# Kernel optimization log

Measured on AMD Instinct MI355X. Metric: run time of the kernel, lower is better.

Reference implementation:

```python
import jax, jax.numpy as jnp
import numpy as np

B, S, IN, H, D, M, OUT = 1, 4096, 2048, 2048, 1024, 65536, 2048
TOP_K = 3
EPS = 1e-12  # F.normalize eps


def setup_inputs() -> dict:
    key = jax.random.key(0)
    ks = jax.random.split(key, 13)
    def g(k, shape, scale):
        return jax.random.normal(k, shape, dtype=jnp.float32) * scale
    return {
        "x": g(ks[0], (B, S, IN), 1.0),
        "W1": g(ks[1], (IN, H), (1.0 / IN) ** 0.5),
        "b1": g(ks[2], (H,), 0.01),
        "W2": g(ks[3], (H, H), (1.0 / H) ** 0.5),
        "b2": g(ks[4], (H,), 0.01),
        "Wq": g(ks[5], (H, D), (1.0 / H) ** 0.5),
        "bq": g(ks[6], (D,), 0.01),
        "Wout": g(ks[7], (H + D, OUT), (1.0 / (H + D)) ** 0.5),
        "bout": g(ks[8], (OUT,), 0.01),
        "keys": g(ks[9], (M, D), 1.0),
        "values": g(ks[10], (M, D), 1.0),
        "importance": jax.random.uniform(ks[11], (M,), dtype=jnp.float32),
    }


def _l2norm(v):
    n = jnp.sqrt(jnp.sum(v * v, axis=-1, keepdims=True))
    return v / jnp.maximum(n, EPS)


def reference(x, W1, b1, W2, b2, Wq, bq, Wout, bout, keys, values, importance):
    # controller: Linear -> ReLU -> Linear over flattened tokens
    h = jnp.maximum(x.reshape(-1, IN) @ W1 + b1, 0.0) @ W2 + b2  # [B*S, H]
    h = h.reshape(B, S, H)
    last_hidden = h[:, -1, :]                                    # [B=1, H]
    # query generation + cosine similarity against memory keys
    q = last_hidden @ Wq + bq                                    # [1, D]
    qn = _l2norm(q)
    kn = _l2norm(keys)                                           # [M, D]
    sims = (qn @ kn.T)[0]                                        # [M]
    weighted = sims * importance                                 # [M]
    top_vals, top_idx = jax.lax.top_k(weighted, TOP_K)
    attn = jax.nn.softmax(top_vals)                              # [K]
    retrieved = attn @ values[top_idx]                           # [D]
    combined = jnp.concatenate([last_hidden, retrieved[None, :]], axis=-1)  # [1, H+D]
    out = combined @ Wout + bout                                 # [1, OUT]
    return out
```

## Files before the change

### kernel.cpp

```cpp
#include <hip/hip_runtime.h>

#define FEPS 1e-12f

template<int RELU>
__global__ void gemv_atomic4(const float* __restrict__ v,
                             const float* __restrict__ W,
                             const float* __restrict__ bias,
                             float* __restrict__ out,
                             int C, int chunk) {
    int j = (blockIdx.x * 256 + threadIdx.x) * 4;
    int i0 = blockIdx.y * chunk;
    float4 acc = make_float4(0.f, 0.f, 0.f, 0.f);
    for (int i = i0; i < i0 + chunk; ++i) {
        float vi = v[i];
        if (RELU) vi = fmaxf(vi, 0.f);
        float4 w = *(const float4*)(W + (size_t)i * C + j);
        acc.x += vi * w.x; acc.y += vi * w.y;
        acc.z += vi * w.z; acc.w += vi * w.w;
    }
    if (blockIdx.y == 0) {
        float4 b = *(const float4*)(bias + j);
        acc.x += b.x; acc.y += b.y; acc.z += b.z; acc.w += b.w;
    }
    atomicAdd(&out[j + 0], acc.x);
    atomicAdd(&out[j + 1], acc.y);
    atomicAdd(&out[j + 2], acc.z);
    atomicAdd(&out[j + 3], acc.w);
}

__global__ void sims_top3(const float* __restrict__ q,
                          const float* __restrict__ keys,
                          const float* __restrict__ imp,
                          float* __restrict__ cand_val,
                          int* __restrict__ cand_idx) {
    __shared__ float qs[1024];
    __shared__ float wv[4 * 3];
    __shared__ int   wi[4 * 3];
    int t = threadIdx.x;
    #pragma unroll
    for (int p = 0; p < 4; ++p) qs[t + 256 * p] = q[t + 256 * p];
    __syncthreads();
    int wave = t >> 6, lane = t & 63;
    const float4* q4 = (const float4*)qs;
    float4 qv[4];
    #pragma unroll
    for (int p = 0; p < 4; ++p) qv[p] = q4[lane + 64 * p];

    float v0 = -INFINITY, v1 = -INFINITY, v2 = -INFINITY;
    int   i0 = -1, i1 = -1, i2 = -1;
    int mbase = blockIdx.x * 64 + wave * 16;
    for (int r = 0; r < 16; ++r) {
        int m = mbase + r;
        const float4* krow = (const float4*)(keys + (size_t)m * 1024);
        float dot = 0.f, sq = 0.f;
        #pragma unroll
        for (int p = 0; p < 4; ++p) {
            float4 k = krow[lane + 64 * p];
            dot += k.x * qv[p].x + k.y * qv[p].y + k.z * qv[p].z + k.w * qv[p].w;
            sq  += k.x * k.x + k.y * k.y + k.z * k.z + k.w * k.w;
        }
        #pragma unroll
        for (int off = 32; off; off >>= 1) {
            dot += __shfl_down(dot, off);
            sq  += __shfl_down(sq, off);
        }
        if (lane == 0) {
            float val = dot * imp[m] / fmaxf(sqrtf(sq), FEPS);
            if (val > v0)      { v2 = v1; i2 = i1; v1 = v0; i1 = i0; v0 = val; i0 = m; }
            else if (val > v1) { v2 = v1; i2 = i1; v1 = val; i1 = m; }
            else if (val > v2) { v2 = val; i2 = m; }
        }
    }
    if (lane == 0) {
        wv[wave * 3 + 0] = v0; wv[wave * 3 + 1] = v1; wv[wave * 3 + 2] = v2;
        wi[wave * 3 + 0] = i0; wi[wave * 3 + 1] = i1; wi[wave * 3 + 2] = i2;
    }
    __syncthreads();
    if (t == 0) {
        float a0 = -INFINITY, a1 = -INFINITY, a2 = -INFINITY;
        int   b0 = -1, b1 = -1, b2 = -1;
        for (int e = 0; e < 12; ++e) {
            float val = wv[e]; int idx = wi[e];
            if (val > a0)      { a2 = a1; b2 = b1; a1 = a0; b1 = b0; a0 = val; b0 = idx; }
            else if (val > a1) { a2 = a1; b2 = b1; a1 = val; b1 = idx; }
            else if (val > a2) { a2 = val; b2 = idx; }
        }
        cand_val[blockIdx.x * 3 + 0] = a0; cand_idx[blockIdx.x * 3 + 0] = b0;
        cand_val[blockIdx.x * 3 + 1] = a1; cand_idx[blockIdx.x * 3 + 1] = b1;
        cand_val[blockIdx.x * 3 + 2] = a2; cand_idx[blockIdx.x * 3 + 2] = b2;
    }
}

__global__ void finalize_retrieve(const float* __restrict__ q,
                                  const float* __restrict__ cand_val,
                                  const int* __restrict__ cand_idx,
                                  const float* __restrict__ values,
                                  float* __restrict__ retrieved) {
    __shared__ float red[1024];
    __shared__ float mv[3 * 1024];
    __shared__ int   mi[3 * 1024];
    __shared__ float s_attn[3];
    __shared__ int   s_idx[3];
    __shared__ float s_qden;
    int t = threadIdx.x;

    float qv = q[t];
    red[t] = qv * qv;
    __syncthreads();
    for (int s = 512; s > 0; s >>= 1) {
        if (t < s) red[t] += red[t + s];
        __syncthreads();
    }
    if (t == 0) s_qden = fmaxf(sqrtf(red[0]), FEPS);

    float v0 = -INFINITY, v1 = -INFINITY, v2 = -INFINITY;
    int   i0 = -1, i1 = -1, i2 = -1;
    #pragma unroll
    for (int k = 0; k < 3; ++k) {
        int c = t + (k << 10);
        float val = cand_val[c];
        int   idx = cand_idx[c];
        if (val > v0)      { v2 = v1; i2 = i1; v1 = v0; i1 = i0; v0 = val; i0 = idx; }
        else if (val > v1) { v2 = v1; i2 = i1; v1 = val; i1 = idx; }
        else if (val > v2) { v2 = val; i2 = idx; }
    }
    mv[t * 3 + 0] = v0; mv[t * 3 + 1] = v1; mv[t * 3 + 2] = v2;
    mi[t * 3 + 0] = i0; mi[t * 3 + 1] = i1; mi[t * 3 + 2] = i2;
    __syncthreads();

    for (int s = 512; s > 0; s >>= 1) {
        if (t < s) {
            float a0 = mv[t * 3], a1 = mv[t * 3 + 1], a2 = mv[t * 3 + 2];
            int   b0 = mi[t * 3], b1 = mi[t * 3 + 1], b2 = mi[t * 3 + 2];
            #pragma unroll
            for (int e = 0; e < 3; ++e) {
                float val = mv[(t + s) * 3 + e];
                int   idx = mi[(t + s) * 3 + e];
                if (val > a0)      { a2 = a1; b2 = b1; a1 = a0; b1 = b0; a0 = val; b0 = idx; }
                else if (val > a1) { a2 = a1; b2 = b1; a1 = val; b1 = idx; }
                else if (val > a2) { a2 = val; b2 = idx; }
            }
            mv[t * 3] = a0; mv[t * 3 + 1] = a1; mv[t * 3 + 2] = a2;
            mi[t * 3] = b0; mi[t * 3 + 1] = b1; mi[t * 3 + 2] = b2;
        }
        __syncthreads();
    }

    if (t == 0) {
        float qden = s_qden;
        float tv0 = mv[0] / qden, tv1 = mv[1] / qden, tv2 = mv[2] / qden;
        float mx = fmaxf(tv0, fmaxf(tv1, tv2));
        float e0 = expf(tv0 - mx), e1 = expf(tv1 - mx), e2 = expf(tv2 - mx);
        float sum = e0 + e1 + e2;
        s_attn[0] = e0 / sum; s_attn[1] = e1 / sum; s_attn[2] = e2 / sum;
        s_idx[0] = mi[0]; s_idx[1] = mi[1]; s_idx[2] = mi[2];
    }
    __syncthreads();

    float r = 0.0f;
    #pragma unroll
    for (int e = 0; e < 3; ++e)
        r += s_attn[e] * values[(size_t)s_idx[e] * 1024 + t];
    retrieved[t] = r;
}

extern "C" void kernel_launch(void* const* d_in, const int* in_sizes, int n_in,
                              void* d_out, int out_size, void* d_ws, size_t ws_size,
                              hipStream_t stream) {
    const float* x      = (const float*)d_in[0];
    const float* W1     = (const float*)d_in[1];
    const float* b1     = (const float*)d_in[2];
    const float* W2     = (const float*)d_in[3];
    const float* b2     = (const float*)d_in[4];
    const float* Wq     = (const float*)d_in[5];
    const float* bq     = (const float*)d_in[6];
    const float* Wout   = (const float*)d_in[7];
    const float* bout   = (const float*)d_in[8];
    const float* keys   = (const float*)d_in[9];
    const float* values = (const float*)d_in[10];
    const float* imp    = (const float*)d_in[11];
    float* out = (float*)d_out;
    float* ws  = (float*)d_ws;

    float* h1       = ws;
    float* comb     = ws + 2048;
    float* retr     = ws + 4096;
    float* q        = ws + 5120;
    float* cand_val = ws + 6144;
    int*   cand_idx = (int*)(ws + 9216);

    const float* xlast = x + (size_t)(4096 - 1) * 2048;

    hipMemsetAsync(d_ws, 0, 6144 * sizeof(float), stream);
    hipMemsetAsync(d_out, 0, (size_t)out_size * sizeof(float), stream);

    gemv_atomic4<0><<<dim3(2, 128), 256, 0, stream>>>(xlast, W1, b1, h1, 2048, 16);
    gemv_atomic4<1><<<dim3(2, 128), 256, 0, stream>>>(h1, W2, b2, comb, 2048, 16);
    gemv_atomic4<0><<<dim3(1, 128), 256, 0, stream>>>(comb, Wq, bq, q, 1024, 16);
    sims_top3<<<1024, 256, 0, stream>>>(q, keys, imp, cand_val, cand_idx);
    finalize_retrieve<<<1, 1024, 0, stream>>>(q, cand_val, cand_idx, values, retr);
    gemv_atomic4<0><<<dim3(2, 128), 256, 0, stream>>>(comb, Wout, bout, out, 2048, 24);
}
```

Measured before the change: 610.5 us.

## Fuse top-3 finalize into sims kernel via last-block counter, retune GEMV splits

Merges the separate single-block finalize/retrieve kernel into the similarity kernel: each block publishes its top-3 candidates, and the last block to finish (found with an atomic ticket counter) does the global top-3 merge, softmax, value gather and zeroing of the output buffer. This drops one kernel launch and one memset. The GEMV kernels now use a compile-time unrolled chunk with twice as many row-split blocks, and the key scan processes four rows at a time for more loads in flight. The cost is extra atomics and fences, and a serial tail on the last block.

After: 701.9 us. 1.15x slower.

```diff
diff --git a/kernel.cpp b/kernel.cpp
--- a/kernel.cpp
+++ b/kernel.cpp
@@ -2,21 +2,34 @@
 
 #define FEPS 1e-12f
 
-template<int RELU>
-__global__ void gemv_atomic4(const float* __restrict__ v,
-                             const float* __restrict__ W,
-                             const float* __restrict__ bias,
-                             float* __restrict__ out,
-                             int C, int chunk) {
+__device__ __forceinline__ void top3_insert(float val, int idx,
+                                            float& v0, float& v1, float& v2,
+                                            int& i0, int& i1, int& i2) {
+    if (val > v0)      { v2 = v1; i2 = i1; v1 = v0; i1 = i0; v0 = val; i0 = idx; }
+    else if (val > v1) { v2 = v1; i2 = i1; v1 = val; i1 = idx; }
+    else if (val > v2) { v2 = val; i2 = idx; }
+}
+
+template<int RELU, int CHUNK>
+__global__ __launch_bounds__(256)
+void gemv_atomic4(const float* __restrict__ v,
+                  const float* __restrict__ W,
+                  const float* __restrict__ bias,
+                  float* __restrict__ out,
+                  int C) {
     int j = (blockIdx.x * 256 + threadIdx.x) * 4;
-    int i0 = blockIdx.y * chunk;
+    int i0 = blockIdx.y * CHUNK;
     float4 acc = make_float4(0.f, 0.f, 0.f, 0.f);
-    for (int i = i0; i < i0 + chunk; ++i) {
+    #pragma unroll
+    for (int u = 0; u < CHUNK; ++u) {
+        int i = i0 + u;
         float vi = v[i];
         if (RELU) vi = fmaxf(vi, 0.f);
         float4 w = *(const float4*)(W + (size_t)i * C + j);
-        acc.x += vi * w.x; acc.y += vi * w.y;
-        acc.z += vi * w.z; acc.w += vi * w.w;
+        acc.x = fmaf(vi, w.x, acc.x);
+        acc.y = fmaf(vi, w.y, acc.y);
+        acc.z = fmaf(vi, w.z, acc.z);
+        acc.w = fmaf(vi, w.w, acc.w);
     }
     if (blockIdx.y == 0) {
         float4 b = *(const float4*)(bias + j);
@@ -28,14 +41,23 @@
     atomicAdd(&out[j + 3], acc.w);
 }
 
-__global__ void sims_top3(const float* __restrict__ q,
-                          const float* __restrict__ keys,
-                          const float* __restrict__ imp,
-                          float* __restrict__ cand_val,
-                          int* __restrict__ cand_idx) {
+__global__ __launch_bounds__(256)
+void sims_top3_fused(const float* __restrict__ q,
+                     const float* __restrict__ keys,
+                     const float* __restrict__ imp,
+                     const float* __restrict__ values,
+                     float* __restrict__ cand_val,
+                     int* __restrict__ cand_idx,
+                     unsigned* __restrict__ ctr,
+                     float* __restrict__ retr,
+                     float* __restrict__ out) {
     __shared__ float qs[1024];
     __shared__ float wv[4 * 3];
     __shared__ int   wi[4 * 3];
+    __shared__ float s_red[4];
+    __shared__ float s_attn[3];
+    __shared__ int   s_idx[3];
+    __shared__ int   s_last;
     int t = threadIdx.x;
     #pragma unroll
     for (int p = 0; p < 4; ++p) qs[t + 256 * p] = q[t + 256 * p];
@@ -49,26 +71,40 @@
     float v0 = -INFINITY, v1 = -INFINITY, v2 = -INFINITY;
     int   i0 = -1, i1 = -1, i2 = -1;
     int mbase = blockIdx.x * 64 + wave * 16;
-    for (int r = 0; r < 16; ++r) {
-        int m = mbase + r;
-        const float4* krow = (const float4*)(keys + (size_t)m * 1024);
-        float dot = 0.f, sq = 0.f;
+    for (int r = 0; r < 16; r += 4) {
+        float dot[4] = {0.f, 0.f, 0.f, 0.f};
+        float sq[4]  = {0.f, 0.f, 0.f, 0.f};
         #pragma unroll
-        for (int p = 0; p < 4; ++p) {
-            float4 k = krow[lane + 64 * p];
-            dot += k.x * qv[p].x + k.y * qv[p].y + k.z * qv[p].z + k.w * qv[p].w;
-            sq  += k.x * k.x + k.y * k.y + k.z * k.z + k.w * k.w;
+        for (int u = 0; u < 4; ++u) {
+            const float4* krow = (const float4*)(keys + (size_t)(mbase + r + u) * 1024);
+            #pragma unroll
+            for (int p = 0; p < 4; ++p) {
+                float4 k = krow[lane + 64 * p];
+                dot[u] = fmaf(k.x, qv[p].x, dot[u]);
+                dot[u] = fmaf(k.y, qv[p].y, dot[u]);
+                dot[u] = fmaf(k.z, qv[p].z, dot[u]);
+                dot[u] = fmaf(k.w, qv[p].w, dot[u]);
+                sq[u]  = fmaf(k.x, k.x, sq[u]);
+                sq[u]  = fmaf(k.y, k.y, sq[u]);
+                sq[u]  = fmaf(k.z, k.z, sq[u]);
+                sq[u]  = fmaf(k.w, k.w, sq[u]);
+            }
         }
         #pragma unroll
         for (int off = 32; off; off >>= 1) {
-            dot += __shfl_down(dot, off);
-            sq  += __shfl_down(sq, off);
+            #pragma unroll
+            for (int u = 0; u < 4; ++u) {
+                dot[u] += __shfl_down(dot[u], off);
+                sq[u]  += __shfl_down(sq[u], off);
+            }
         }
         if (lane == 0) {
-            float val = dot * imp[m] / fmaxf(sqrtf(sq), FEPS);
-            if (val > v0)      { v2 = v1; i2 = i1; v1 = v0; i1 = i0; v0 = val; i0 = m; }
-            else if (val > v1) { v2 = v1; i2 = i1; v1 = val; i1 = m; }
-            else if (val > v2) { v2 = val; i2 = m; }
+            #pragma unroll
+            for (int u = 0; u < 4; ++u) {
+                int m = mbase + r + u;
+                float val = dot[u] * imp[m] / fmaxf(sqrtf(sq[u]), FEPS);
+                top3_insert(val, m, v0, v1, v2, i0, i1, i2);
+            }
         }
     }
     if (lane == 0) {
@@ -79,89 +115,77 @@
     if (t == 0) {
         float a0 = -INFINITY, a1 = -INFINITY, a2 = -INFINITY;
         int   b0 = -1, b1 = -1, b2 = -1;
-        for (int e = 0; e < 12; ++e) {
-            float val = wv[e]; int idx = wi[e];
-            if (val > a0)      { a2 = a1; b2 = b1; a1 = a0; b1 = b0; a0 = val; b0 = idx; }
-            else if (val > a1) { a2 = a1; b2 = b1; a1 = val; b1 = idx; }
-            else if (val > a2) { a2 = val; b2 = idx; }
-        }
-        cand_val[blockIdx.x * 3 + 0] = a0; cand_idx[blockIdx.x * 3 + 0] = b0;
-        cand_val[blockIdx.x * 3 + 1] = a1; cand_idx[blockIdx.x * 3 + 1] = b1;
-        cand_val[blockIdx.x * 3 + 2] = a2; cand_idx[blockIdx.x * 3 + 2] = b2;
-    }
-}
-
-__global__ void finalize_retrieve(const float* __restrict__ q,
-                                  const float* __restrict__ cand_val,
-                                  const int* __restrict__ cand_idx,
-                                  const float* __restrict__ values,
-                                  float* __restrict__ retrieved) {
-    __shared__ float red[1024];
-    __shared__ float mv[3 * 1024];
-    __shared__ int   mi[3 * 1024];
-    __shared__ float s_attn[3];
-    __shared__ int   s_idx[3];
-    __shared__ float s_qden;
-    int t = threadIdx.x;
-
-    float qv = q[t];
-    red[t] = qv * qv;
-    __syncthreads();
-    for (int s = 512; s > 0; s >>= 1) {
-        if (t < s) red[t] += red[t + s];
-        __syncthreads();
-    }
-    if (t == 0) s_qden = fmaxf(sqrtf(red[0]), FEPS);
-
-    float v0 = -INFINITY, v1 = -INFINITY, v2 = -INFINITY;
-    int   i0 = -1, i1 = -1, i2 = -1;
-    #pragma unroll
-    for (int k = 0; k < 3; ++k) {
-        int c = t + (k << 10);
-        float val = cand_val[c];
-        int   idx = cand_idx[c];
-        if (val > v0)      { v2 = v1; i2 = i1; v1 = v0; i1 = i0; v0 = val; i0 = idx; }
-        else if (val > v1) { v2 = v1; i2 = i1; v1 = val; i1 = idx; }
-        else if (val > v2) { v2 = val; i2 = idx; }
-    }
-    mv[t * 3 + 0] = v0; mv[t * 3 + 1] = v1; mv[t * 3 + 2] = v2;
-    mi[t * 3 + 0] = i0; mi[t * 3 + 1] = i1; mi[t * 3 + 2] = i2;
-    __syncthreads();
-
-    for (int s = 512; s > 0; s >>= 1) {
-        if (t < s) {
-            float a0 = mv[t * 3], a1 = mv[t * 3 + 1], a2 = mv[t * 3 + 2];
-            int   b0 = mi[t * 3], b1 = mi[t * 3 + 1], b2 = mi[t * 3 + 2];
-            #pragma unroll
-            for (int e = 0; e < 3; ++e) {
-                float val = mv[(t + s) * 3 + e];
-                int   idx = mi[(t + s) * 3 + e];
-                if (val > a0)      { a2 = a1; b2 = b1; a1 = a0; b1 = b0; a0 = val; b0 = idx; }
-                else if (val > a1) { a2 = a1; b2 = b1; a1 = val; b1 = idx; }
-                else if (val > a2) { a2 = val; b2 = idx; }
-            }
-            mv[t * 3] = a0; mv[t * 3 + 1] = a1; mv[t * 3 + 2] = a2;
-            mi[t * 3] = b0; mi[t * 3 + 1] = b1; mi[t * 3 + 2] = b2;
-        }
-        __syncthreads();
-    }
-
+        for (int e = 0; e < 12; ++e)
+            top3_insert(wv[e], wi[e], a0, a1, a2, b0, b1, b2);
+        int base = blockIdx.x * 3;
+        __hip_atomic_store(&cand_val[base + 0], a0, __ATOMIC_RELAXED, __HIP_MEMORY_SCOPE_AGENT);
+        __hip_atomic_store(&cand_val[base + 1], a1, __ATOMIC_RELAXED, __HIP_MEMORY_SCOPE_AGENT);
+        __hip_atomic_store(&cand_val[base + 2], a2, __ATOMIC_RELAXED, __HIP_MEMORY_SCOPE_AGENT);
+        __hip_atomic_store(&cand_idx[base + 0], b0, __ATOMIC_RELAXED, __HIP_MEMORY_SCOPE_AGENT);
+        __hip_atomic_store(&cand_idx[base + 1], b1, __ATOMIC_RELAXED, __HIP_MEMORY_SCOPE_AGENT);
+        __hip_atomic_store(&cand_idx[base + 2], b2, __ATOMIC_RELAXED, __HIP_MEMORY_SCOPE_AGENT);
+        __threadfence();
+        unsigned tk = __hip_atomic_fetch_add(ctr, 1u, __ATOMIC_ACQ_REL, __HIP_MEMORY_SCOPE_AGENT);
+        s_last = (tk == gridDim.x - 1) ? 1 : 0;
+    }
+    __syncthreads();
+    if (!s_last) return;
+
+    __threadfence();
+    float pq = 0.f;
+    #pragma unroll
+    for (int p = 0; p < 4; ++p) { float x = qs[t + 256 * p]; pq = fmaf(x, x, pq); }
+    #pragma unroll
+    for (int off = 32; off; off >>= 1) pq += __shfl_down(pq, off);
+
+    float c0 = -INFINITY, c1 = -INFINITY, c2 = -INFINITY;
+    int   d0 = -1, d1 = -1, d2 = -1;
+    #pragma unroll
+    for (int kk = 0; kk < 12; ++kk) {
+        int c = t + (kk << 8);
+        float val = __hip_atomic_load(&cand_val[c], __ATOMIC_RELAXED, __HIP_MEMORY_SCOPE_AGENT);
+        int   idx = __hip_atomic_load(&cand_idx[c], __ATOMIC_RELAXED, __HIP_MEMORY_SCOPE_AGENT);
+        top3_insert(val, idx, c0, c1, c2, d0, d1, d2);
+    }
+    #pragma unroll
+    for (int off = 32; off; off >>= 1) {
+        float u0 = __shfl_down(c0, off), u1 = __shfl_down(c1, off), u2 = __shfl_down(c2, off);
+        int   j0 = __shfl_down(d0, off), j1 = __shfl_down(d1, off), j2 = __shfl_down(d2, off);
+        top3_insert(u0, j0, c0, c1, c2, d0, d1, d2);
+        top3_insert(u1, j1, c0, c1, c2, d0, d1, d2);
+        top3_insert(u2, j2, c0, c1, c2, d0, d1, d2);
+    }
+    if (lane == 0) {
+        wv[wave * 3 + 0] = c0; wv[wave * 3 + 1] = c1; wv[wave * 3 + 2] = c2;
+        wi[wave * 3 + 0] = d0; wi[wave * 3 + 1] = d1; wi[wave * 3 + 2] = d2;
+        s_red[wave] = pq;
+    }
+    __syncthreads();
     if (t == 0) {
-        float qden = s_qden;
-        float tv0 = mv[0] / qden, tv1 = mv[1] / qden, tv2 = mv[2] / qden;
+        float a0 = -INFINITY, a1 = -INFINITY, a2 = -INFINITY;
+        int   b0 = -1, b1 = -1, b2 = -1;
+        for (int e = 0; e < 12; ++e)
+            top3_insert(wv[e], wi[e], a0, a1, a2, b0, b1, b2);
+        float qden = fmaxf(sqrtf(s_red[0] + s_red[1] + s_red[2] + s_red[3]), FEPS);
+        float tv0 = a0 / qden, tv1 = a1 / qden, tv2 = a2 / qden;
         float mx = fmaxf(tv0, fmaxf(tv1, tv2));
         float e0 = expf(tv0 - mx), e1 = expf(tv1 - mx), e2 = expf(tv2 - mx);
         float sum = e0 + e1 + e2;
         s_attn[0] = e0 / sum; s_attn[1] = e1 / sum; s_attn[2] = e2 / sum;
-        s_idx[0] = mi[0]; s_idx[1] = mi[1]; s_idx[2] = mi[2];
-    }
-    __syncthreads();
-
-    float r = 0.0f;
-    #pragma unroll
-    for (int e = 0; e < 3; ++e)
-        r += s_attn[e] * values[(size_t)s_idx[e] * 1024 + t];
-    retrieved[t] = r;
+        s_idx[0] = b0; s_idx[1] = b1; s_idx[2] = b2;
+    }
+    __syncthreads();
+
+    #pragma unroll
+    for (int p = 0; p < 4; ++p) {
+        int col = t + 256 * p;
+        float r = s_attn[0] * values[(size_t)s_idx[0] * 1024 + col]
+                + s_attn[1] * values[(size_t)s_idx[1] * 1024 + col]
+                + s_attn[2] * values[(size_t)s_idx[2] * 1024 + col];
+        retr[col] = r;
+    }
+    #pragma unroll
+    for (int p = 0; p < 8; ++p) out[t + 256 * p] = 0.0f;
 }
 
 extern "C" void kernel_launch(void* const* d_in, const int* in_sizes, int n_in,
@@ -182,22 +206,22 @@
     float* out = (float*)d_out;
     float* ws  = (float*)d_ws;
 
-    float* h1       = ws;
-    float* comb     = ws + 2048;
-    float* retr     = ws + 4096;
-    float* q        = ws + 5120;
-    float* cand_val = ws + 6144;
-    int*   cand_idx = (int*)(ws + 9216);
+    float*    h1       = ws;
+    float*    comb     = ws + 2048;
+    float*    retr     = ws + 4096;
+    float*    q        = ws + 5120;
+    unsigned* ctr      = (unsigned*)(ws + 6144);
+    float*    cand_val = ws + 6160;
+    int*      cand_idx = (int*)(ws + 9232);
 
     const float* xlast = x + (size_t)(4096 - 1) * 2048;
 
-    hipMemsetAsync(d_ws, 0, 6144 * sizeof(float), stream);
-    hipMemsetAsync(d_out, 0, (size_t)out_size * sizeof(float), stream);
-
-    gemv_atomic4<0><<<dim3(2, 128), 256, 0, stream>>>(xlast, W1, b1, h1, 2048, 16);
-    gemv_atomic4<1><<<dim3(2, 128), 256, 0, stream>>>(h1, W2, b2, comb, 2048, 16);
-    gemv_atomic4<0><<<dim3(1, 128), 256, 0, stream>>>(comb, Wq, bq, q, 1024, 16);
-    sims_top3<<<1024, 256, 0, stream>>>(q, keys, imp, cand_val, cand_idx);
-    finalize_retrieve<<<1, 1024, 0, stream>>>(q, cand_val, cand_idx, values, retr);
-    gemv_atomic4<0><<<dim3(2, 128), 256, 0, stream>>>(comb, Wout, bout, out, 2048, 24);
-}
+    hipMemsetAsync(d_ws, 0, 6160 * sizeof(float), stream);
+
+    gemv_atomic4<0, 8><<<dim3(2, 256), 256, 0, stream>>>(xlast, W1, b1, h1, 2048);
+    gemv_atomic4<1, 8><<<dim3(2, 256), 256, 0, stream>>>(h1, W2, b2, comb, 2048);
+    gemv_atomic4<0, 8><<<dim3(1, 256), 256, 0, stream>>>(comb, Wq, bq, q, 1024);
+    sims_top3_fused<<<1024, 256, 0, stream>>>(q, keys, imp, values,
+                                              cand_val, cand_idx, ctr, retr, out);
+    gemv_atomic4<0, 12><<<dim3(2, 256), 256, 0, stream>>>(comb, Wout, bout, out, 2048);
+}
```
